# Kernel optimization log

Hardware: AMD Instinct MI355X
Metric: run time of the kernel (lower is better)

The kernel has to match this reference:

```python
import jax, jax.numpy as jnp
import numpy as np

N = 25600            # 64 graphs x 400 ROIs
F_IN = 400
H = 128
E = 512000           # 8000 edges per graph
B = 64
G = 8
OUT = 2
NPG = 400            # nodes per graph
EPG = E // B         # edges per graph
BN_EPS = 1e-5


def _xavier(k, shape):
    lim = float(np.sqrt(6.0 / (shape[0] + shape[1])))
    return jax.random.uniform(k, shape, jnp.float32, -lim, lim)


def setup_inputs() -> dict:
    key = jax.random.key(0)
    ks = jax.random.split(key, 16)
    inp = {}
    inp["x"] = jax.random.normal(ks[0], (N, F_IN), jnp.float32)
    # within-graph random edges: local index + graph offset
    src_l = jax.random.randint(ks[1], (E,), 0, NPG, jnp.int32)
    dst_l = jax.random.randint(ks[2], (E,), 0, NPG, jnp.int32)
    off = (jnp.arange(E, dtype=jnp.int32) // EPG) * NPG
    inp["edge_index"] = jnp.stack([src_l + off, dst_l + off])
    inp["batch"] = (jnp.arange(N, dtype=jnp.int32) // NPG)
    inp["group_ids"] = jax.random.randint(ks[3], (N,), 0, G, jnp.int32)
    inp["ge"] = _xavier(ks[4], (G, 2))
    inp["he"] = _xavier(ks[5], (2, 2))
    dims = [(F_IN + 4, H), (H, H), (H, H)]
    for i, (di, do) in enumerate(dims):
        k1, k2 = jax.random.split(ks[6 + i])
        inp[f"w{i}a"] = _xavier(k1, (di, do))
        inp[f"b{i}a"] = jnp.zeros((do,), jnp.float32)
        inp[f"g{i}"] = jnp.ones((do,), jnp.float32)
        inp[f"be{i}"] = jnp.zeros((do,), jnp.float32)
        inp[f"w{i}b"] = _xavier(k2, (do, do))
        inp[f"b{i}b"] = jnp.zeros((do,), jnp.float32)
    inp["wfa"] = _xavier(ks[10], (H, H))
    inp["bfa"] = jnp.zeros((H,), jnp.float32)
    inp["wfb"] = _xavier(ks[11], (H, OUT))
    inp["bfb"] = jnp.zeros((OUT,), jnp.float32)
    return inp


def _bn(h, gamma, beta):
    # BatchNorm1d in training mode: stats over node dimension
    mu = jnp.mean(h, axis=0, keepdims=True)
    var = jnp.var(h, axis=0, keepdims=True)
    return gamma * (h - mu) * jax.lax.rsqrt(var + BN_EPS) + beta


def reference(x, edge_index, batch, group_ids, ge, he,
              w0a, b0a, g0, be0, w0b, b0b,
              w1a, b1a, g1, be1, w1b, b1b,
              w2a, b2a, g2, be2, w2b, b2b,
              wfa, bfa, wfb, bfb):
    n = x.shape[0]
    hemi = jnp.arange(n) % 2                      # [1::2] = 1
    h = jnp.concatenate([x, ge[group_ids], he[hemi]], axis=-1)  # [N, F_IN+4]
    src, dst = edge_index[0], edge_index[1]
    layers = [(w0a, b0a, g0, be0, w0b, b0b),
              (w1a, b1a, g1, be1, w1b, b1b),
              (w2a, b2a, g2, be2, w2b, b2b)]
    for wa, ba, g, be, wb, bb in layers:
        # GINConv (eps=0): x_i + sum_{(j,i)} x_j, then 2-layer MLP w/ batchnorm
        agg = jax.ops.segment_sum(h[src], dst, num_segments=N)
        z = h + agg
        z = jax.nn.relu(_bn(z @ wa + ba, g, be))  # dropout = identity (eval)
        h = jax.nn.relu(z @ wb + bb)              # outer ReLU from forward()
    pooled = jax.ops.segment_sum(h, batch, num_segments=B)  # global_add_pool
    return jax.nn.relu(pooled @ wfa + bfa) @ wfb + bfb
```

## Files before the change

kernel.cpp:

```cpp
#include <hip/hip_runtime.h>

#define N_NODES 25600
#define F_IN 400
#define NE 512000
#define NB 64
#define NPG 400
#define EPG 8000
#define BN_EPS 1e-5f
#define NBLK 256

typedef __attribute__((ext_vector_type(8))) short short8;
typedef __attribute__((ext_vector_type(4))) float floatx4;
typedef unsigned short us;
typedef unsigned long long u64;

__device__ __forceinline__ unsigned short f2bf(float f) {
    unsigned int u = __float_as_uint(f);
    u += 0x7FFF + ((u >> 16) & 1);
    return (unsigned short)(u >> 16);
}
__device__ __forceinline__ float bf2f(unsigned short s) {
    return __uint_as_float((unsigned int)s << 16);
}
__device__ __forceinline__ short u8bf(unsigned v) {
    return (short)(__float_as_uint((float)v) >> 16);
}
__device__ __forceinline__ void ast64(void* p, u64 v) {
    __hip_atomic_store((u64*)p, v, __ATOMIC_RELAXED, __HIP_MEMORY_SCOPE_AGENT);
}
__device__ __forceinline__ u64 pk4(unsigned short a, unsigned short b, unsigned short c, unsigned short d) {
    return (u64)a | ((u64)b << 16) | ((u64)c << 32) | ((u64)d << 48);
}

__device__ __forceinline__ void gsync_tree(unsigned* bar, int bid, int phase) {
    __syncthreads();
    if (threadIdx.x == 0) {
        unsigned* leaf = bar + 32 + (bid >> 4) * 32;
        unsigned v = __hip_atomic_fetch_add(leaf, 1u, __ATOMIC_RELAXED, __HIP_MEMORY_SCOPE_AGENT);
        if (v == (unsigned)(phase * 16 - 1))
            __hip_atomic_fetch_add(bar, 1u, __ATOMIC_RELAXED, __HIP_MEMORY_SCOPE_AGENT);
        while (__hip_atomic_load(bar, __ATOMIC_RELAXED, __HIP_MEMORY_SCOPE_AGENT) < (unsigned)(phase * 16))
            __builtin_amdgcn_s_sleep(16);
        asm volatile("" ::: "memory");
    }
    __syncthreads();
}

__device__ __forceinline__ void gbar4(unsigned* gc, int stage) {
    __syncthreads();
    if (threadIdx.x == 0) {
        __hip_atomic_fetch_add(gc, 1u, __ATOMIC_RELAXED, __HIP_MEMORY_SCOPE_AGENT);
        while (__hip_atomic_load(gc, __ATOMIC_RELAXED, __HIP_MEMORY_SCOPE_AGENT) < (unsigned)(stage * 4))
            __builtin_amdgcn_s_sleep(8);
        asm volatile("" ::: "memory");
    }
    __syncthreads();
}



__device__ __forceinline__ void ph_prep(unsigned char* sm, int g, int q, int bid, int tid,
        const int* __restrict__ src, const int* __restrict__ dst, us* __restrict__ SbBF,
        const float* __restrict__ wa0, const float* __restrict__ wa1, const float* __restrict__ wa2,
        const float* __restrict__ wb0, const float* __restrict__ wb1, const float* __restrict__ wb2,
        us* __restrict__ wt0, us* __restrict__ wtb0, us* __restrict__ wta1,
        us* __restrict__ wtb1, us* __restrict__ wta2, us* __restrict__ wtb2,
        float* __restrict__ pstat, us* __restrict__ tT0, us* __restrict__ tT1, us* __restrict__ tT2) {
    int r0 = q * 112;
    int* cnt = (int*)sm;
    for (int i = tid; i < 11200; i += 1024) cnt[i] = 0;
    __syncthreads();
    int ebase = g * EPG, nbase = g * NPG;
    for (int e = tid; e < EPG; e += 1024) {
        int d = dst[ebase + e] - nbase;
        int dr = d - r0;
        if ((unsigned)dr < 112u) {
            int s = src[ebase + e] - nbase;
            int idx = dr * NPG + s;
            atomicAdd(&cnt[idx >> 2], (int)(1u << ((idx & 3) * 8)));
        }
    }
    __syncthreads();
    const unsigned char* cb = (const unsigned char*)cnt;
    for (int i = tid; i < 112 * 112; i += 1024) {
        int rr = i / 112, c4 = (i % 112) * 4;
        int R = r0 + rr;
        ushort4 o;
#pragma unroll
        for (int j = 0; j < 4; ++j) {
            int c = c4 + j;
            unsigned v = (R < NPG && c < NPG) ? (unsigned)cb[rr * NPG + c] + (c == R ? 1u : 0u) : 0u;
            ((unsigned short*)&o)[j] = (unsigned short)u8bf(v);
        }
        *(ushort4*)&SbBF[((size_t)g * 512 + R) * 448 + c4] = o;
    }
    if (q == 3) {
        for (int i = tid; i < 64 * 112; i += 1024) {
            int rr = 448 + i / 112, c4 = (i % 112) * 4;
            *(u64*)&SbBF[((size_t)g * 512 + rr) * 448 + c4] = 0ull;
        }
    }
    if (bid < 64) {
        int idx = bid * 1024 + tid;
        if (idx < 14336) {
            int n = idx / 112, k0 = (idx % 112) * 4;
            unsigned short o[4];
#pragma unroll
            for (int j = 0; j < 4; ++j) {
                int k = k0 + j;
                o[j] = (k < 400) ? f2bf(wa0[(size_t)k * 128 + n]) : (unsigned short)0;
            }
            ast64(&wt0[(size_t)n * 448 + k0], pk4(o[0], o[1], o[2], o[3]));
        } else if (idx < 34816) {
            int r2 = idx - 14336;
            int m = r2 >> 12, qi = r2 & 4095;
            int r = qi * 4, n = r >> 7, k = r & 127;
            const float* smat = (m == 0) ? wb0 : (m == 1) ? wa1 : (m == 2) ? wb1 : (m == 3) ? wa2 : wb2;
            us* dmat = (m == 0) ? wtb0 : (m == 1) ? wta1 : (m == 2) ? wtb1 : (m == 3) ? wta2 : wtb2;
            unsigned short o[4];
#pragma unroll
            for (int j = 0; j < 4; ++j) o[j] = f2bf(smat[(size_t)(k + j) * 128 + n]);
            ast64(&dmat[r], pk4(o[0], o[1], o[2], o[3]));
        } else if (idx < 45056) {
            int qi = idx - 34816;
            ast64(&((u64*)pstat)[qi], 0ull);
        } else if (idx < 45440) {
            int qi = idx - 45056;
            us* t = (qi < 128) ? tT0 : (qi < 256) ? tT1 : tT2;
            ast64(&t[(size_t)128 * N_NODES + (qi & 127) * 4], 0ull);
        }
    }
}


__device__ __forceinline__ void ph_embed(unsigned char* sm, int g, int q, int tid,
        const float* __restrict__ x, const us* __restrict__ wt0, const float* __restrict__ wa0,
        const int* __restrict__ gid, const float* __restrict__ ge, const float* __restrict__ he,
        us* __restrict__ tTw) {
    us (*Bf)[456] = (us(*)[456])sm;
    us (*As)[72] = (us(*)[72])(sm + 116736);
    float (*Wex)[128] = (float(*)[128])(sm + 135168);
    int nb = g * NPG + q * 100;
    int wave = tid >> 6, lane = tid & 63;
    int wrow = wave >> 2, wc4 = wave & 3;
    int fm = lane & 15, quad = lane >> 4;

    for (int i = tid; i < 7168; i += 1024) {
        int col = i / 56, kq = (i % 56) * 8;
        *(short8*)&Bf[col][kq] = *(const short8*)(wt0 + (size_t)col * 448 + kq);
    }
    for (int i = tid; i < 512; i += 1024)
        Wex[i >> 7][i & 127] = wa0[(size_t)(400 + (i >> 7)) * 128 + (i & 127)];

    floatx4 acc[2][2];
#pragma unroll
    for (int rt = 0; rt < 2; ++rt)
#pragma unroll
        for (int ct = 0; ct < 2; ++ct) acc[rt][ct] = (floatx4){0.f, 0.f, 0.f, 0.f};

    const int rA = tid >> 3, kcA = (tid & 7) * 8;
    float v[8];
    auto loadK = [&](int ks) {
        int kg = ks * 64 + kcA;
        if (rA < 100) {
            const float* ar = x + (size_t)(nb + rA) * F_IN;
            if (kg + 7 < 400) {
                float4 a = *(const float4*)(ar + kg);
                float4 b = *(const float4*)(ar + kg + 4);
                v[0] = a.x; v[1] = a.y; v[2] = a.z; v[3] = a.w;
                v[4] = b.x; v[5] = b.y; v[6] = b.z; v[7] = b.w;
            } else {
#pragma unroll
                for (int j = 0; j < 8; ++j) v[j] = (kg + j < 400) ? ar[kg + j] : 0.f;
            }
        } else {
#pragma unroll
            for (int j = 0; j < 8; ++j) v[j] = 0.f;
        }
    };

    loadK(0);
    for (int ks = 0; ks < 7; ++ks) {
        {
            short8 s;
#pragma unroll
            for (int j = 0; j < 8; ++j) s[j] = (short)f2bf(v[j]);
            *(short8*)&As[rA][kcA] = s;
        }
        __syncthreads();
        if (ks + 1 < 7) loadK(ks + 1);
#pragma unroll
        for (int k0l = 0; k0l < 64; k0l += 32) {
            short8 af[2], bf[2];
#pragma unroll
            for (int rt = 0; rt < 2; ++rt)
                af[rt] = *(const short8*)&As[wrow * 32 + rt * 16 + fm][k0l + quad * 8];
#pragma unroll
            for (int ct = 0; ct < 2; ++ct)
                bf[ct] = *(const short8*)&Bf[wc4 * 32 + ct * 16 + fm][ks * 64 + k0l + quad * 8];
#pragma unroll
            for (int rt = 0; rt < 2; ++rt)
#pragma unroll
                for (int ct = 0; ct < 2; ++ct)
                    acc[rt][ct] = __builtin_amdgcn_mfma_f32_16x16x32_bf16(
                        af[rt], bf[ct], acc[rt][ct], 0, 0, 0);
        }
        __syncthreads();
    }

#pragma unroll
    for (int rt = 0; rt < 2; ++rt)
#pragma unroll
        for (int ct = 0; ct < 2; ++ct) {
            int col = wc4 * 32 + ct * 16 + fm;
            int rl0 = wrow * 32 + rt * 16 + quad * 4;
            if (rl0 < 100) {
                unsigned short o[4];
#pragma unroll
                for (int r = 0; r < 4; ++r) {
                    int row = nb + rl0 + r;
                    int gv = gid[row];
                    float vv = acc[rt][ct][r]
                             + ge[gv * 2] * Wex[0][col] + ge[gv * 2 + 1] * Wex[1][col]
                             + he[(row & 1) * 2] * Wex[2][col] + he[(row & 1) * 2 + 1] * Wex[3][col];
                    o[r] = f2bf(vv);
                }
                ast64(&tTw[(size_t)col * N_NODES + nb + rl0], pk4(o[0], o[1], o[2], o[3]));
            }
        }
}


__device__ __forceinline__ void ph_agg(unsigned char* sm, int g, int q, int tid,
        const us* __restrict__ SbBF, const us* __restrict__ tTr, const float* __restrict__ ba,
        float* __restrict__ psum, float* __restrict__ psq, int bucket) {
    us (*Bf)[456] = (us(*)[456])sm;
    us (*zl)[136] = (us(*)[136])sm;
    float (*rs)[4][2][16] = (float(*)[4][2][16])(sm + 116736);
    float (*rq)[4][2][16] = (float(*)[4][2][16])(sm + 118784);
    int wave = tid >> 6, lane = tid & 63;
    int wrow = wave >> 2, wc4 = wave & 3;
    int fm = lane & 15, quad = lane >> 4;
    int node0 = g * NPG;

    for (int i = tid; i < 7168; i += 1024) {
        int col = i / 56, kq = (i % 56) * 8;
        *(short8*)&Bf[col][kq] = *(const short8*)(tTr + (size_t)col * N_NODES + node0 + kq);
    }
    __syncthreads();

    floatx4 acc[2][2];
#pragma unroll
    for (int rt = 0; rt < 2; ++rt)
#pragma unroll
        for (int ct = 0; ct < 2; ++ct) acc[rt][ct] = (floatx4){0.f, 0.f, 0.f, 0.f};

    const us* abase = SbBF + ((size_t)g * 512 + q * 112) * 448;
#pragma unroll
    for (int ks = 0; ks < 7; ++ks) {
#pragma unroll
        for (int k0l = 0; k0l < 64; k0l += 32) {
            short8 af[2], bf[2];
#pragma unroll
            for (int rt = 0; rt < 2; ++rt)
                af[rt] = *(const short8*)(abase + (size_t)(wrow * 32 + rt * 16 + fm) * 448
                                          + ks * 64 + k0l + quad * 8);
#pragma unroll
            for (int ct = 0; ct < 2; ++ct)
                bf[ct] = *(const short8*)&Bf[wc4 * 32 + ct * 16 + fm][ks * 64 + k0l + quad * 8];
#pragma unroll
            for (int rt = 0; rt < 2; ++rt)
#pragma unroll
                for (int ct = 0; ct < 2; ++ct)
                    acc[rt][ct] = __builtin_amdgcn_mfma_f32_16x16x32_bf16(
                        af[rt], bf[ct], acc[rt][ct], 0, 0, 0);
        }
    }
    __syncthreads();

    int nrows = (q < 3) ? 112 : 64;
    float sc[2] = {0.f, 0.f}, sq2[2] = {0.f, 0.f};
#pragma unroll
    for (int rt = 0; rt < 2; ++rt)
#pragma unroll
        for (int ct = 0; ct < 2; ++ct) {
            int col = wc4 * 32 + ct * 16 + fm;
            int rl0 = wrow * 32 + rt * 16 + quad * 4;
            if (rl0 < nrows) {
                float bv = ba[col];
#pragma unroll
                for (int r = 0; r < 4; ++r) {
                    float vv = acc[rt][ct][r] + bv;
                    zl[rl0 + r][col] = f2bf(vv);
                    sc[ct] += vv;
                    sq2[ct] += vv * vv;
                }
            }
        }
#pragma unroll
    for (int ct = 0; ct < 2; ++ct) {
        sc[ct] += __shfl_xor(sc[ct], 16);
        sc[ct] += __shfl_xor(sc[ct], 32);
        sq2[ct] += __shfl_xor(sq2[ct], 16);
        sq2[ct] += __shfl_xor(sq2[ct], 32);
    }
    if (lane < 16) {
#pragma unroll
        for (int ct = 0; ct < 2; ++ct) { rs[wrow][wc4][ct][lane] = sc[ct]; rq[wrow][wc4][ct][lane] = sq2[ct]; }
    }
    __syncthreads();
    if (tid < 128) {
        int wc = tid >> 5, ct = (tid >> 4) & 1, f = tid & 15;
        float S = 0.f, Q = 0.f;
#pragma unroll
        for (int wr = 0; wr < 4; ++wr) { S += rs[wr][wc][ct][f]; Q += rq[wr][wc][ct][f]; }
        atomicAdd(&psum[bucket * 128 + tid], S);
        atomicAdd(&psq[bucket * 128 + tid], Q);
    }
}


template <int FINAL>
__device__ __forceinline__ void ph_post(unsigned char* sm, int g, int q, int tid,
        const float* __restrict__ psum, const float* __restrict__ psq,
        const float* __restrict__ gamma, const float* __restrict__ beta,
        const us* __restrict__ wtb, const float* __restrict__ bb,
        const us* __restrict__ wta_next, us* __restrict__ tTw, float& p0, float& p1) {
    us (*zl)[136] = (us(*)[136])sm;
    float* coefs = (float*)(sm + 34816);
    us (*hs)[136] = (us(*)[136])(sm + 35840);
    us (*Bw)[72] = (us(*)[72])(sm + 70656);
    int wave = tid >> 6, lane = tid & 63;
    int wrow = wave >> 2, wc4 = wave & 3;
    int fm = lane & 15, quad = lane >> 4;
    int nrows = (q < 3) ? 112 : 64;
    int nb = g * NPG + q * 112;

    if (tid < 128) {
        float S = 0.f, Q = 0.f;
#pragma unroll
        for (int b = 0; b < 16; ++b) {
            S += __hip_atomic_load(&psum[b * 128 + tid], __ATOMIC_RELAXED, __HIP_MEMORY_SCOPE_AGENT);
            Q += __hip_atomic_load(&psq[b * 128 + tid], __ATOMIC_RELAXED, __HIP_MEMORY_SCOPE_AGENT);
        }
        float invn = 1.0f / (float)N_NODES;
        float mu = S * invn;
        float var = Q * invn - mu * mu;
        float a = gamma[tid] * rsqrtf(var + BN_EPS);
        coefs[tid] = a;
        coefs[128 + tid] = beta[tid] - a * mu;
    }
    __syncthreads();
    for (int i = tid; i < 16384; i += 1024) {
        int rl = i >> 7, col = i & 127;
        float vv = bf2f(zl[rl][col]);
        zl[rl][col] = f2bf(fmaxf(coefs[col] * vv + coefs[128 + col], 0.f));
    }
    __syncthreads();

    floatx4 acc[2][2];
#pragma unroll
    for (int rt = 0; rt < 2; ++rt)
#pragma unroll
        for (int ct = 0; ct < 2; ++ct) acc[rt][ct] = (floatx4){0.f, 0.f, 0.f, 0.f};

    const int nB = tid >> 3, kc = (tid & 7) * 8;
    for (int ks = 0; ks < 2; ++ks) {
        *(short8*)&Bw[nB][kc] = *(const short8*)(wtb + (size_t)nB * 128 + ks * 64 + kc);
        __syncthreads();
#pragma unroll
        for (int k0l = 0; k0l < 64; k0l += 32) {
            short8 af[2], bf[2];
#pragma unroll
            for (int rt = 0; rt < 2; ++rt)
                af[rt] = *(const short8*)&zl[wrow * 32 + rt * 16 + fm][ks * 64 + k0l + quad * 8];
#pragma unroll
            for (int ct = 0; ct < 2; ++ct)
                bf[ct] = *(const short8*)&Bw[wc4 * 32 + ct * 16 + fm][k0l + quad * 8];
#pragma unroll
            for (int rt = 0; rt < 2; ++rt)
#pragma unroll
                for (int ct = 0; ct < 2; ++ct)
                    acc[rt][ct] = __builtin_amdgcn_mfma_f32_16x16x32_bf16(
                        af[rt], bf[ct], acc[rt][ct], 0, 0, 0);
        }
        __syncthreads();
    }

    if (FINAL) {
#pragma unroll
        for (int rt = 0; rt < 2; ++rt)
#pragma unroll
            for (int ct = 0; ct < 2; ++ct) {
                int col = wc4 * 32 + ct * 16 + fm;
                int rl0 = wrow * 32 + rt * 16 + quad * 4;
                if (rl0 < nrows) {
                    float bv = bb[col];
                    float s = 0.f;
#pragma unroll
                    for (int r = 0; r < 4; ++r) s += fmaxf(acc[rt][ct][r] + bv, 0.f);
                    if (ct == 0) p0 += s; else p1 += s;
                }
            }
        return;
    }

#pragma unroll
    for (int rt = 0; rt < 2; ++rt)
#pragma unroll
        for (int ct = 0; ct < 2; ++ct) {
            int col = wc4 * 32 + ct * 16 + fm;
            float bv = bb[col];
            int rl0 = wrow * 32 + rt * 16 + quad * 4;
#pragma unroll
            for (int r = 0; r < 4; ++r)
                hs[rl0 + r][col] = f2bf(fmaxf(acc[rt][ct][r] + bv, 0.f));
        }
    __syncthreads();

#pragma unroll
    for (int rt = 0; rt < 2; ++rt)
#pragma unroll
        for (int ct = 0; ct < 2; ++ct) acc[rt][ct] = (floatx4){0.f, 0.f, 0.f, 0.f};

    for (int ks = 0; ks < 2; ++ks) {
        *(short8*)&Bw[nB][kc] = *(const short8*)(wta_next + (size_t)nB * 128 + ks * 64 + kc);
        __syncthreads();
#pragma unroll
        for (int k0l = 0; k0l < 64; k0l += 32) {
            short8 af[2], bf[2];
#pragma unroll
            for (int rt = 0; rt < 2; ++rt)
                af[rt] = *(const short8*)&hs[wrow * 32 + rt * 16 + fm][ks * 64 + k0l + quad * 8];
#pragma unroll
            for (int ct = 0; ct < 2; ++ct)
                bf[ct] = *(const short8*)&Bw[wc4 * 32 + ct * 16 + fm][k0l + quad * 8];
#pragma unroll
            for (int rt = 0; rt < 2; ++rt)
#pragma unroll
                for (int ct = 0; ct < 2; ++ct)
                    acc[rt][ct] = __builtin_amdgcn_mfma_f32_16x16x32_bf16(
                        af[rt], bf[ct], acc[rt][ct], 0, 0, 0);
        }
        __syncthreads();
    }

#pragma unroll
    for (int rt = 0; rt < 2; ++rt)
#pragma unroll
        for (int ct = 0; ct < 2; ++ct) {
            int col = wc4 * 32 + ct * 16 + fm;
            int rl0 = wrow * 32 + rt * 16 + quad * 4;
            if (rl0 < nrows) {
                unsigned short o[4];
#pragma unroll
                for (int r = 0; r < 4; ++r) o[r] = f2bf(acc[rt][ct][r]);
                ast64(&tTw[(size_t)col * N_NODES + nb + rl0], pk4(o[0], o[1], o[2], o[3]));
            }
        }
}


__global__ __launch_bounds__(1024, 4) void persist_all(
        const float* __restrict__ x, const int* __restrict__ esrc, const int* __restrict__ edst,
        const int* __restrict__ gid, const float* __restrict__ ge, const float* __restrict__ he,
        const float* __restrict__ wa0, const float* __restrict__ ba0, const float* __restrict__ gg0,
        const float* __restrict__ be0, const float* __restrict__ wb0, const float* __restrict__ bbias0,
        const float* __restrict__ wa1, const float* __restrict__ ba1, const float* __restrict__ gg1,
        const float* __restrict__ be1, const float* __restrict__ wb1, const float* __restrict__ bbias1,
        const float* __restrict__ wa2, const float* __restrict__ ba2, const float* __restrict__ gg2,
        const float* __restrict__ be2, const float* __restrict__ wb2, const float* __restrict__ bbias2,
        const float* __restrict__ wfa, const float* __restrict__ bfa,
        const float* __restrict__ wfb, const float* __restrict__ bfb,
        us* __restrict__ tT0, us* __restrict__ tT1, us* __restrict__ tT2,
        us* __restrict__ SbBF, float* __restrict__ pstat,
        us* __restrict__ wt0, us* __restrict__ wtb0, us* __restrict__ wta1,
        us* __restrict__ wtb1, us* __restrict__ wta2, us* __restrict__ wtb2,
        unsigned* __restrict__ bar, float* __restrict__ out) {
    __shared__ __align__(16) unsigned char sm[137216];
    int bid = blockIdx.x, tid = threadIdx.x;
    int g = (bid & 7) * 8 + ((bid >> 3) & 7);
    int q = bid >> 6;
    unsigned* gc = bar + 544 + g * 32;
    float* pooled = pstat + 12288;
    float p0 = 0.f, p1 = 0.f;

    ph_prep(sm, g, q, bid, tid, esrc, edst, SbBF, wa0, wa1, wa2, wb0, wb1, wb2,
            wt0, wtb0, wta1, wtb1, wta2, wtb2, pstat, tT0, tT1, tT2);
    gsync_tree(bar, bid, 1);
    ph_embed(sm, g, q, tid, x, wt0, wa0, gid, ge, he, tT0);
    gbar4(gc, 1);

    ph_agg(sm, g, q, tid, SbBF, tT0, ba0, pstat + 0, pstat + 2048, bid & 15);
    gsync_tree(bar, bid, 2);
    ph_post<0>(sm, g, q, tid, pstat + 0, pstat + 2048, gg0, be0, wtb0, bbias0, wta1, tT1, p0, p1);
    gbar4(gc, 2);

    ph_agg(sm, g, q, tid, SbBF, tT1, ba1, pstat + 4096, pstat + 6144, bid & 15);
    gsync_tree(bar, bid, 3);
    ph_post<0>(sm, g, q, tid, pstat + 4096, pstat + 6144, gg1, be1, wtb1, bbias1, wta2, tT2, p0, p1);
    gbar4(gc, 3);

    ph_agg(sm, g, q, tid, SbBF, tT2, ba2, pstat + 8192, pstat + 10240, bid & 15);
    gsync_tree(bar, bid, 4);
    ph_post<1>(sm, g, q, tid, pstat + 8192, pstat + 10240, gg2, be2, wtb2, bbias2, nullptr, nullptr, p0, p1);

    {
        int wave = tid >> 6, lane = tid & 63;
        int wrow = wave >> 2, wc4 = wave & 3;
        float (*red)[4][2][16] = (float(*)[4][2][16])sm;
        p0 += __shfl_xor(p0, 16); p0 += __shfl_xor(p0, 32);
        p1 += __shfl_xor(p1, 16); p1 += __shfl_xor(p1, 32);
        __syncthreads();
        if (lane < 16) { red[wrow][wc4][0][lane] = p0; red[wrow][wc4][1][lane] = p1; }
        __syncthreads();
        if (tid < 128) {
            int wc = tid >> 5, ct = (tid >> 4) & 1, f = tid & 15;
            float s = 0.f;
#pragma unroll
            for (int wr = 0; wr < 4; ++wr) s += red[wr][wc][ct][f];
            atomicAdd(&pooled[g * 128 + tid], s);
        }
    }
    gbar4(gc, 4);

    if (q == 0) {
        float* pl = (float*)sm;
        float* o0 = pl + 128;
        float* o1 = pl + 256;
        __syncthreads();
        if (tid < 128) {
            unsigned uv = __hip_atomic_load((const unsigned*)&pooled[g * 128 + tid],
                                            __ATOMIC_RELAXED, __HIP_MEMORY_SCOPE_AGENT);
            pl[tid] = __uint_as_float(uv);
        }
        __syncthreads();
        if (tid < 128) {
            float a = bfa[tid];
            for (int k = 0; k < 128; ++k) a += pl[k] * wfa[k * 128 + tid];
            float p2 = fmaxf(a, 0.f);
            o0[tid] = p2 * wfb[tid * 2 + 0];
            o1[tid] = p2 * wfb[tid * 2 + 1];
        }
        __syncthreads();
        if (tid == 0) {
            float a0 = bfb[0], a1 = bfb[1];
#pragma unroll
            for (int k = 0; k < 128; ++k) { a0 += o0[k]; a1 += o1[k]; }
            out[g * 2 + 0] = a0;
            out[g * 2 + 1] = a1;
        }
    }
}


extern "C" void kernel_launch(void* const* d_in, const int* in_sizes, int n_in,
                              void* d_out, int out_size, void* d_ws, size_t ws_size,
                              hipStream_t stream) {
    const float* x   = (const float*)d_in[0];
    const int* ei    = (const int*)d_in[1];
    const int* gid   = (const int*)d_in[3];
    const float* ge  = (const float*)d_in[4];
    const float* he  = (const float*)d_in[5];
    float* out = (float*)d_out;

    char* ws = (char*)d_ws;
    size_t o = 0;
    auto alloc = [&](size_t bytes) { char* p = ws + o; o += (bytes + 255) & ~(size_t)255; return p; };
    size_t tbytes = ((size_t)128 * N_NODES + 512) * 2;
    us* tT0 = (us*)alloc(tbytes);
    us* tT1 = (us*)alloc(tbytes);
    us* tT2 = (us*)alloc(tbytes);
    us* SbBF = (us*)alloc((size_t)NB * 512 * 448 * 2);
    float* pstat = (float*)alloc(20480 * 4);
    us* wt0  = (us*)alloc(128 * 448 * 2);
    us* wtb0 = (us*)alloc(128 * 128 * 2);
    us* wta1 = (us*)alloc(128 * 128 * 2);
    us* wtb1 = (us*)alloc(128 * 128 * 2);
    us* wta2 = (us*)alloc(128 * 128 * 2);
    us* wtb2 = (us*)alloc(128 * 128 * 2);
    unsigned* bar = (unsigned*)alloc(12288);
    (void)ws_size; (void)in_sizes; (void)n_in; (void)out_size;

    hipMemsetAsync(bar, 0, 12288, stream);

    persist_all<<<NBLK, 1024, 0, stream>>>(
        x, ei, ei + NE, gid, ge, he,
        (const float*)d_in[6],  (const float*)d_in[7],  (const float*)d_in[8],
        (const float*)d_in[9],  (const float*)d_in[10], (const float*)d_in[11],
        (const float*)d_in[12], (const float*)d_in[13], (const float*)d_in[14],
        (const float*)d_in[15], (const float*)d_in[16], (const float*)d_in[17],
        (const float*)d_in[18], (const float*)d_in[19], (const float*)d_in[20],
        (const float*)d_in[21], (const float*)d_in[22], (const float*)d_in[23],
        (const float*)d_in[24], (const float*)d_in[25],
        (const float*)d_in[26], (const float*)d_in[27],
        tT0, tT1, tT2, SbBF, pstat, wt0, wtb0, wta1, wtb1, wta2, wtb2,
        bar, out);
}
```

Baseline: 244.6 us.

## Remove prep phase and grid barrier by converting weights per block in LDS

Drops the separate prep phase and its grid-wide tree barrier. Each block now transposes and converts the fp32 weights to bf16 straight into LDS during the embed and post phases, and builds its adjacency slice after the embed, synchronised only by the per-graph barrier. Stats and barrier counters are zeroed by a host memset, padding rows are dropped from the adjacency buffer, and out-of-range aggregation columns are zero-filled in registers. The cost is redundant per-block weight conversion and strided global reads, in exchange for one fewer global sync.

```diff
diff --git a/kernel.cpp b/kernel.cpp
--- a/kernel.cpp
+++ b/kernel.cpp
@@ -40,7 +40,7 @@
         if (v == (unsigned)(phase * 16 - 1))
             __hip_atomic_fetch_add(bar, 1u, __ATOMIC_RELAXED, __HIP_MEMORY_SCOPE_AGENT);
         while (__hip_atomic_load(bar, __ATOMIC_RELAXED, __HIP_MEMORY_SCOPE_AGENT) < (unsigned)(phase * 16))
-            __builtin_amdgcn_s_sleep(16);
+            __builtin_amdgcn_s_sleep(8);
         asm volatile("" ::: "memory");
     }
     __syncthreads();
@@ -59,84 +59,10 @@
 
 
 
-__device__ __forceinline__ void ph_prep(unsigned char* sm, int g, int q, int bid, int tid,
-        const int* __restrict__ src, const int* __restrict__ dst, us* __restrict__ SbBF,
-        const float* __restrict__ wa0, const float* __restrict__ wa1, const float* __restrict__ wa2,
-        const float* __restrict__ wb0, const float* __restrict__ wb1, const float* __restrict__ wb2,
-        us* __restrict__ wt0, us* __restrict__ wtb0, us* __restrict__ wta1,
-        us* __restrict__ wtb1, us* __restrict__ wta2, us* __restrict__ wtb2,
-        float* __restrict__ pstat, us* __restrict__ tT0, us* __restrict__ tT1, us* __restrict__ tT2) {
-    int r0 = q * 112;
-    int* cnt = (int*)sm;
-    for (int i = tid; i < 11200; i += 1024) cnt[i] = 0;
-    __syncthreads();
-    int ebase = g * EPG, nbase = g * NPG;
-    for (int e = tid; e < EPG; e += 1024) {
-        int d = dst[ebase + e] - nbase;
-        int dr = d - r0;
-        if ((unsigned)dr < 112u) {
-            int s = src[ebase + e] - nbase;
-            int idx = dr * NPG + s;
-            atomicAdd(&cnt[idx >> 2], (int)(1u << ((idx & 3) * 8)));
-        }
-    }
-    __syncthreads();
-    const unsigned char* cb = (const unsigned char*)cnt;
-    for (int i = tid; i < 112 * 112; i += 1024) {
-        int rr = i / 112, c4 = (i % 112) * 4;
-        int R = r0 + rr;
-        ushort4 o;
-#pragma unroll
-        for (int j = 0; j < 4; ++j) {
-            int c = c4 + j;
-            unsigned v = (R < NPG && c < NPG) ? (unsigned)cb[rr * NPG + c] + (c == R ? 1u : 0u) : 0u;
-            ((unsigned short*)&o)[j] = (unsigned short)u8bf(v);
-        }
-        *(ushort4*)&SbBF[((size_t)g * 512 + R) * 448 + c4] = o;
-    }
-    if (q == 3) {
-        for (int i = tid; i < 64 * 112; i += 1024) {
-            int rr = 448 + i / 112, c4 = (i % 112) * 4;
-            *(u64*)&SbBF[((size_t)g * 512 + rr) * 448 + c4] = 0ull;
-        }
-    }
-    if (bid < 64) {
-        int idx = bid * 1024 + tid;
-        if (idx < 14336) {
-            int n = idx / 112, k0 = (idx % 112) * 4;
-            unsigned short o[4];
-#pragma unroll
-            for (int j = 0; j < 4; ++j) {
-                int k = k0 + j;
-                o[j] = (k < 400) ? f2bf(wa0[(size_t)k * 128 + n]) : (unsigned short)0;
-            }
-            ast64(&wt0[(size_t)n * 448 + k0], pk4(o[0], o[1], o[2], o[3]));
-        } else if (idx < 34816) {
-            int r2 = idx - 14336;
-            int m = r2 >> 12, qi = r2 & 4095;
-            int r = qi * 4, n = r >> 7, k = r & 127;
-            const float* smat = (m == 0) ? wb0 : (m == 1) ? wa1 : (m == 2) ? wb1 : (m == 3) ? wa2 : wb2;
-            us* dmat = (m == 0) ? wtb0 : (m == 1) ? wta1 : (m == 2) ? wtb1 : (m == 3) ? wta2 : wtb2;
-            unsigned short o[4];
-#pragma unroll
-            for (int j = 0; j < 4; ++j) o[j] = f2bf(smat[(size_t)(k + j) * 128 + n]);
-            ast64(&dmat[r], pk4(o[0], o[1], o[2], o[3]));
-        } else if (idx < 45056) {
-            int qi = idx - 34816;
-            ast64(&((u64*)pstat)[qi], 0ull);
-        } else if (idx < 45440) {
-            int qi = idx - 45056;
-            us* t = (qi < 128) ? tT0 : (qi < 256) ? tT1 : tT2;
-            ast64(&t[(size_t)128 * N_NODES + (qi & 127) * 4], 0ull);
-        }
-    }
-}
-
-
 __device__ __forceinline__ void ph_embed(unsigned char* sm, int g, int q, int tid,
-        const float* __restrict__ x, const us* __restrict__ wt0, const float* __restrict__ wa0,
+        const float* __restrict__ x, const float* __restrict__ wa0,
         const int* __restrict__ gid, const float* __restrict__ ge, const float* __restrict__ he,
-        us* __restrict__ tTw) {
+        us* __restrict__ tT0) {
     us (*Bf)[456] = (us(*)[456])sm;
     us (*As)[72] = (us(*)[72])(sm + 116736);
     float (*Wex)[128] = (float(*)[128])(sm + 135168);
@@ -145,9 +71,13 @@
     int wrow = wave >> 2, wc4 = wave & 3;
     int fm = lane & 15, quad = lane >> 4;
 
-    for (int i = tid; i < 7168; i += 1024) {
-        int col = i / 56, kq = (i % 56) * 8;
-        *(short8*)&Bf[col][kq] = *(const short8*)(wt0 + (size_t)col * 448 + kq);
+    for (int i = tid; i < 51200; i += 1024) {
+        int k = i >> 7, n = i & 127;
+        Bf[n][k] = f2bf(wa0[i]);
+    }
+    for (int i = tid; i < 6144; i += 1024) {
+        int k = 400 + (i >> 7), n = i & 127;
+        Bf[n][k] = 0;
     }
     for (int i = tid; i < 512; i += 1024)
         Wex[i >> 7][i & 127] = wa0[(size_t)(400 + (i >> 7)) * 128 + (i & 127)];
@@ -225,9 +155,43 @@
                              + he[(row & 1) * 2] * Wex[2][col] + he[(row & 1) * 2 + 1] * Wex[3][col];
                     o[r] = f2bf(vv);
                 }
-                ast64(&tTw[(size_t)col * N_NODES + nb + rl0], pk4(o[0], o[1], o[2], o[3]));
+                ast64(&tT0[(size_t)col * N_NODES + nb + rl0], pk4(o[0], o[1], o[2], o[3]));
             }
         }
+}
+
+
+__device__ __forceinline__ void ph_prepadj(unsigned char* sm, int g, int q, int tid,
+        const int* __restrict__ src, const int* __restrict__ dst, us* __restrict__ SbBF) {
+    int r0 = q * 112;
+    int* cnt = (int*)sm;
+    __syncthreads();
+    for (int i = tid; i < 11200; i += 1024) cnt[i] = 0;
+    __syncthreads();
+    int ebase = g * EPG, nbase = g * NPG;
+    for (int e = tid; e < EPG; e += 1024) {
+        int d = dst[ebase + e] - nbase;
+        int dr = d - r0;
+        if ((unsigned)dr < 112u) {
+            int s = src[ebase + e] - nbase;
+            int idx = dr * NPG + s;
+            atomicAdd(&cnt[idx >> 2], (int)(1u << ((idx & 3) * 8)));
+        }
+    }
+    __syncthreads();
+    const unsigned char* cb = (const unsigned char*)cnt;
+    for (int i = tid; i < 112 * 112; i += 1024) {
+        int rr = i / 112, c4 = (i % 112) * 4;
+        int R = r0 + rr;
+        ushort4 o;
+#pragma unroll
+        for (int j = 0; j < 4; ++j) {
+            int c = c4 + j;
+            unsigned v = (R < NPG && c < NPG) ? (unsigned)cb[rr * NPG + c] + (c == R ? 1u : 0u) : 0u;
+            ((unsigned short*)&o)[j] = (unsigned short)u8bf(v);
+        }
+        *(ushort4*)&SbBF[((size_t)g * 448 + R) * 448 + c4] = o;
+    }
 }
 
 
@@ -245,7 +209,10 @@
 
     for (int i = tid; i < 7168; i += 1024) {
         int col = i / 56, kq = (i % 56) * 8;
-        *(short8*)&Bf[col][kq] = *(const short8*)(tTr + (size_t)col * N_NODES + node0 + kq);
+        short8 vv;
+        if (kq < 400) vv = *(const short8*)(tTr + (size_t)col * N_NODES + node0 + kq);
+        else vv = (short8){0, 0, 0, 0, 0, 0, 0, 0};
+        *(short8*)&Bf[col][kq] = vv;
     }
     __syncthreads();
 
@@ -255,7 +222,7 @@
 #pragma unroll
         for (int ct = 0; ct < 2; ++ct) acc[rt][ct] = (floatx4){0.f, 0.f, 0.f, 0.f};
 
-    const us* abase = SbBF + ((size_t)g * 512 + q * 112) * 448;
+    const us* abase = SbBF + ((size_t)g * 448 + q * 112) * 448;
 #pragma unroll
     for (int ks = 0; ks < 7; ++ks) {
 #pragma unroll
@@ -324,12 +291,12 @@
 __device__ __forceinline__ void ph_post(unsigned char* sm, int g, int q, int tid,
         const float* __restrict__ psum, const float* __restrict__ psq,
         const float* __restrict__ gamma, const float* __restrict__ beta,
-        const us* __restrict__ wtb, const float* __restrict__ bb,
-        const us* __restrict__ wta_next, us* __restrict__ tTw, float& p0, float& p1) {
+        const float* __restrict__ wbf, const float* __restrict__ bb,
+        const float* __restrict__ wanf, us* __restrict__ tTw, float& p0, float& p1) {
     us (*zl)[136] = (us(*)[136])sm;
     float* coefs = (float*)(sm + 34816);
     us (*hs)[136] = (us(*)[136])(sm + 35840);
-    us (*Bw)[72] = (us(*)[72])(sm + 70656);
+    us (*Bw)[136] = (us(*)[136])(sm + 70656);
     int wave = tid >> 6, lane = tid & 63;
     int wrow = wave >> 2, wc4 = wave & 3;
     int fm = lane & 15, quad = lane >> 4;
@@ -350,6 +317,10 @@
         coefs[tid] = a;
         coefs[128 + tid] = beta[tid] - a * mu;
     }
+    for (int i = tid; i < 16384; i += 1024) {
+        int k = i >> 7, n = i & 127;
+        Bw[n][k] = f2bf(wbf[i]);
+    }
     __syncthreads();
     for (int i = tid; i < 16384; i += 1024) {
         int rl = i >> 7, col = i & 127;
@@ -364,10 +335,8 @@
 #pragma unroll
         for (int ct = 0; ct < 2; ++ct) acc[rt][ct] = (floatx4){0.f, 0.f, 0.f, 0.f};
 
-    const int nB = tid >> 3, kc = (tid & 7) * 8;
-    for (int ks = 0; ks < 2; ++ks) {
-        *(short8*)&Bw[nB][kc] = *(const short8*)(wtb + (size_t)nB * 128 + ks * 64 + kc);
-        __syncthreads();
+#pragma unroll
+    for (int ks = 0; ks < 2; ++ks)
 #pragma unroll
         for (int k0l = 0; k0l < 64; k0l += 32) {
             short8 af[2], bf[2];
@@ -376,7 +345,7 @@
                 af[rt] = *(const short8*)&zl[wrow * 32 + rt * 16 + fm][ks * 64 + k0l + quad * 8];
 #pragma unroll
             for (int ct = 0; ct < 2; ++ct)
-                bf[ct] = *(const short8*)&Bw[wc4 * 32 + ct * 16 + fm][k0l + quad * 8];
+                bf[ct] = *(const short8*)&Bw[wc4 * 32 + ct * 16 + fm][ks * 64 + k0l + quad * 8];
 #pragma unroll
             for (int rt = 0; rt < 2; ++rt)
 #pragma unroll
@@ -384,8 +353,6 @@
                     acc[rt][ct] = __builtin_amdgcn_mfma_f32_16x16x32_bf16(
                         af[rt], bf[ct], acc[rt][ct], 0, 0, 0);
         }
-        __syncthreads();
-    }
 
     if (FINAL) {
 #pragma unroll
@@ -417,15 +384,19 @@
                 hs[rl0 + r][col] = f2bf(fmaxf(acc[rt][ct][r] + bv, 0.f));
         }
     __syncthreads();
+    for (int i = tid; i < 16384; i += 1024) {
+        int k = i >> 7, n = i & 127;
+        Bw[n][k] = f2bf(wanf[i]);
+    }
+    __syncthreads();
 
 #pragma unroll
     for (int rt = 0; rt < 2; ++rt)
 #pragma unroll
         for (int ct = 0; ct < 2; ++ct) acc[rt][ct] = (floatx4){0.f, 0.f, 0.f, 0.f};
 
-    for (int ks = 0; ks < 2; ++ks) {
-        *(short8*)&Bw[nB][kc] = *(const short8*)(wta_next + (size_t)nB * 128 + ks * 64 + kc);
-        __syncthreads();
+#pragma unroll
+    for (int ks = 0; ks < 2; ++ks)
 #pragma unroll
         for (int k0l = 0; k0l < 64; k0l += 32) {
             short8 af[2], bf[2];
@@ -434,7 +405,7 @@
                 af[rt] = *(const short8*)&hs[wrow * 32 + rt * 16 + fm][ks * 64 + k0l + quad * 8];
 #pragma unroll
             for (int ct = 0; ct < 2; ++ct)
-                bf[ct] = *(const short8*)&Bw[wc4 * 32 + ct * 16 + fm][k0l + quad * 8];
+                bf[ct] = *(const short8*)&Bw[wc4 * 32 + ct * 16 + fm][ks * 64 + k0l + quad * 8];
 #pragma unroll
             for (int rt = 0; rt < 2; ++rt)
 #pragma unroll
@@ -442,8 +413,6 @@
                     acc[rt][ct] = __builtin_amdgcn_mfma_f32_16x16x32_bf16(
                         af[rt], bf[ct], acc[rt][ct], 0, 0, 0);
         }
-        __syncthreads();
-    }
 
 #pragma unroll
     for (int rt = 0; rt < 2; ++rt)
@@ -474,8 +443,6 @@
         const float* __restrict__ wfb, const float* __restrict__ bfb,
         us* __restrict__ tT0, us* __restrict__ tT1, us* __restrict__ tT2,
         us* __restrict__ SbBF, float* __restrict__ pstat,
-        us* __restrict__ wt0, us* __restrict__ wtb0, us* __restrict__ wta1,
-        us* __restrict__ wtb1, us* __restrict__ wta2, us* __restrict__ wtb2,
         unsigned* __restrict__ bar, float* __restrict__ out) {
     __shared__ __align__(16) unsigned char sm[137216];
     int bid = blockIdx.x, tid = threadIdx.x;
@@ -485,25 +452,23 @@
     float* pooled = pstat + 12288;
     float p0 = 0.f, p1 = 0.f;
 
-    ph_prep(sm, g, q, bid, tid, esrc, edst, SbBF, wa0, wa1, wa2, wb0, wb1, wb2,
-            wt0, wtb0, wta1, wtb1, wta2, wtb2, pstat, tT0, tT1, tT2);
+    ph_embed(sm, g, q, tid, x, wa0, gid, ge, he, tT0);
+    ph_prepadj(sm, g, q, tid, esrc, edst, SbBF);
+    gbar4(gc, 1);
+
+    ph_agg(sm, g, q, tid, SbBF, tT0, ba0, pstat + 0, pstat + 2048, bid & 15);
     gsync_tree(bar, bid, 1);
-    ph_embed(sm, g, q, tid, x, wt0, wa0, gid, ge, he, tT0);
-    gbar4(gc, 1);
-
-    ph_agg(sm, g, q, tid, SbBF, tT0, ba0, pstat + 0, pstat + 2048, bid & 15);
+    ph_post<0>(sm, g, q, tid, pstat + 0, pstat + 2048, gg0, be0, wb0, bbias0, wa1, tT1, p0, p1);
+    gbar4(gc, 2);
+
+    ph_agg(sm, g, q, tid, SbBF, tT1, ba1, pstat + 4096, pstat + 6144, bid & 15);
     gsync_tree(bar, bid, 2);
-    ph_post<0>(sm, g, q, tid, pstat + 0, pstat + 2048, gg0, be0, wtb0, bbias0, wta1, tT1, p0, p1);
-    gbar4(gc, 2);
-
-    ph_agg(sm, g, q, tid, SbBF, tT1, ba1, pstat + 4096, pstat + 6144, bid & 15);
+    ph_post<0>(sm, g, q, tid, pstat + 4096, pstat + 6144, gg1, be1, wb1, bbias1, wa2, tT2, p0, p1);
+    gbar4(gc, 3);
+
+    ph_agg(sm, g, q, tid, SbBF, tT2, ba2, pstat + 8192, pstat + 10240, bid & 15);
     gsync_tree(bar, bid, 3);
-    ph_post<0>(sm, g, q, tid, pstat + 4096, pstat + 6144, gg1, be1, wtb1, bbias1, wta2, tT2, p0, p1);
-    gbar4(gc, 3);
-
-    ph_agg(sm, g, q, tid, SbBF, tT2, ba2, pstat + 8192, pstat + 10240, bid & 15);
-    gsync_tree(bar, bid, 4);
-    ph_post<1>(sm, g, q, tid, pstat + 8192, pstat + 10240, gg2, be2, wtb2, bbias2, nullptr, nullptr, p0, p1);
+    ph_post<1>(sm, g, q, tid, pstat + 8192, pstat + 10240, gg2, be2, wb2, bbias2, nullptr, nullptr, p0, p1);
 
     {
         int wave = tid >> 6, lane = tid & 63;
@@ -567,22 +532,16 @@
     char* ws = (char*)d_ws;
     size_t o = 0;
     auto alloc = [&](size_t bytes) { char* p = ws + o; o += (bytes + 255) & ~(size_t)255; return p; };
-    size_t tbytes = ((size_t)128 * N_NODES + 512) * 2;
+    size_t tbytes = (size_t)128 * N_NODES * 2;
     us* tT0 = (us*)alloc(tbytes);
     us* tT1 = (us*)alloc(tbytes);
     us* tT2 = (us*)alloc(tbytes);
-    us* SbBF = (us*)alloc((size_t)NB * 512 * 448 * 2);
+    us* SbBF = (us*)alloc((size_t)NB * 448 * 448 * 2);
     float* pstat = (float*)alloc(20480 * 4);
-    us* wt0  = (us*)alloc(128 * 448 * 2);
-    us* wtb0 = (us*)alloc(128 * 128 * 2);
-    us* wta1 = (us*)alloc(128 * 128 * 2);
-    us* wtb1 = (us*)alloc(128 * 128 * 2);
-    us* wta2 = (us*)alloc(128 * 128 * 2);
-    us* wtb2 = (us*)alloc(128 * 128 * 2);
     unsigned* bar = (unsigned*)alloc(12288);
     (void)ws_size; (void)in_sizes; (void)n_in; (void)out_size;
 
-    hipMemsetAsync(bar, 0, 12288, stream);
+    hipMemsetAsync(pstat, 0, 81920 + 12288, stream);
 
     persist_all<<<NBLK, 1024, 0, stream>>>(
         x, ei, ei + NE, gid, ge, he,
@@ -594,6 +553,5 @@
         (const float*)d_in[21], (const float*)d_in[22], (const float*)d_in[23],
         (const float*)d_in[24], (const float*)d_in[25],
         (const float*)d_in[26], (const float*)d_in[27],
-        tT0, tT1, tT2, SbBF, pstat, wt0, wtb0, wta1, wtb1, wta2, wtb2,
-        bar, out);
-}
+        tT0, tT1, tT2, SbBF, pstat, bar, out);
+}
```

New measurement: 249.0 us. About the same (+1.8%).
